# Kernel optimization log

Measured on AMD Instinct MI355X. Metric: run time of the kernel, lower is better.

The kernel has to match this reference:

```python
import jax, jax.numpy as jnp
import numpy as np

SIZE = 768
SMALL = SIZE // 4 + 1  # 193
N_ROWS = 16 * 512      # 8192 flattened timesteps
N_CODES = 30000
N_PAIRS = 300000


def setup_inputs() -> dict:
    key = jax.random.key(0)
    ks = jax.random.split(key, 10)
    rnn_output = jax.random.normal(ks[0], (16, 512, SIZE), dtype=jnp.float32)
    weight = jax.random.normal(ks[1], (N_CODES, SIZE + 1), dtype=jnp.float32) * 0.02
    weight1 = jax.random.normal(ks[2], (N_CODES, SMALL), dtype=jnp.float32) * 0.02
    idx0 = jnp.stack([
        jax.random.randint(ks[3], (N_PAIRS,), 0, N_ROWS),
        jax.random.randint(ks[4], (N_PAIRS,), 0, N_CODES),
    ], axis=1).astype(jnp.int64)
    y0 = (jax.random.uniform(ks[5], (N_PAIRS,)) < 0.5).astype(jnp.float32)
    idx1 = jnp.stack([
        jax.random.randint(ks[6], (N_PAIRS,), 0, N_ROWS),
        jax.random.randint(ks[7], (N_PAIRS,), 0, N_CODES),
    ], axis=1).astype(jnp.int64)
    y1 = (jax.random.uniform(ks[8], (N_PAIRS,)) < 0.5).astype(jnp.float32)
    seen0 = jnp.zeros((N_PAIRS,), dtype=jnp.float32)
    seen1 = jnp.zeros((N_PAIRS,), dtype=jnp.float32)
    return {"rnn_output": rnn_output, "weight": weight, "weight1": weight1,
            "idx0": idx0, "y0": y0, "seen0": seen0,
            "idx1": idx1, "y1": y1, "seen1": seen1}


def _embedding_dot(features, table, idx):
    # gather feature rows and code-embedding rows, then row-wise dot -> [N]
    f = features[idx[:, 0]]   # [N, D]
    w = table[idx[:, 1]]      # [N, D]
    return jnp.sum(f * w, axis=-1)


def _bce_logits_sum(logits, targets):
    # stable: log(1 + exp(x)) - x*y, summed
    return jnp.sum(jnp.logaddexp(jnp.float32(0.0), logits) - logits * targets)


def reference(rnn_output, weight, weight1, idx0, y0, seen0, idx1, y1, seen1):
    flat = rnn_output.reshape(-1, SIZE)                     # [B*T, size]
    bias = jnp.ones((flat.shape[0], 1), dtype=flat.dtype)
    rnn_with_bias = jnp.concatenate([flat, bias], axis=1)   # [B*T, size+1]

    final = _embedding_dot(rnn_with_bias, weight, idx0)     # [N]
    loss = _bce_logits_sum(final, y0)

    smaller = rnn_with_bias[:, -SMALL:]                     # [B*T, small]
    final1 = _embedding_dot(smaller, weight1, idx1)         # [N]
    loss1 = _bce_logits_sum(final1, y1)

    return final, loss + loss1
```

## Files before the change

kernel.cpp:

```cpp
#include <hip/hip_runtime.h>
#include <hip/hip_fp16.h>

#define FSIZE   768
#define TW0     769
#define TW1     193
#define COL1    576
#define NPAIRS  300000
#define NCODES  30000
#define NROWS   8192
#define W1STRIDE 200
#define NCB     32768
#define NWAVES0 (NPAIRS / 16)
#define NB0     ((NWAVES0 + 3) / 4)
#define NB1     (NPAIRS / 32)
#define NPART   (NB0 + NB1)

#define SZ_FEAT16 (NROWS * FSIZE / 2)
#define SZ_W116   (NCODES * W1STRIDE / 2)

typedef _Float16 h2_t __attribute__((ext_vector_type(2)));

#if defined(__has_builtin)
# if __has_builtin(__builtin_amdgcn_fdot2)
#  define HAVE_FDOT2 1
# endif
#endif

__device__ __forceinline__ float fdot2f(h2_t a, h2_t b, float c) {
#ifdef HAVE_FDOT2
    return __builtin_amdgcn_fdot2(a, b, c, false);
#else
    return (float)a[0] * (float)b[0] + (float)a[1] * (float)b[1] + c;
#endif
}

__device__ __forceinline__ float loss_term(float x, float y) {
    float ax = fabsf(x);
    return fmaxf(x, 0.0f) + log1pf(__expf(-ax)) - x * y;
}

__device__ __forceinline__ float4 ld4u(const float* p) {
    float4 v; __builtin_memcpy(&v, p, 16); return v;
}

__device__ __forceinline__ float acc8(uint4 u, float4 wa, float4 wb, float s) {
    h2_t h0, h1, h2v, h3;
    __builtin_memcpy(&h0, &u.x, 4);
    __builtin_memcpy(&h1, &u.y, 4);
    __builtin_memcpy(&h2v, &u.z, 4);
    __builtin_memcpy(&h3, &u.w, 4);
    s += (float)h0[0] * wa.x; s += (float)h0[1] * wa.y;
    s += (float)h1[0] * wa.z; s += (float)h1[1] * wa.w;
    s += (float)h2v[0] * wb.x; s += (float)h2v[1] * wb.y;
    s += (float)h3[0] * wb.z; s += (float)h3[1] * wb.w;
    return s;
}

__device__ __forceinline__ float dot8hh(uint4 a, uint4 b, float s) {
    h2_t a0, a1, a2, a3, b0, b1, b2, b3;
    __builtin_memcpy(&a0, &a.x, 4); __builtin_memcpy(&a1, &a.y, 4);
    __builtin_memcpy(&a2, &a.z, 4); __builtin_memcpy(&a3, &a.w, 4);
    __builtin_memcpy(&b0, &b.x, 4); __builtin_memcpy(&b1, &b.y, 4);
    __builtin_memcpy(&b2, &b.z, 4); __builtin_memcpy(&b3, &b.w, 4);
    s = fdot2f(a0, b0, s); s = fdot2f(a1, b1, s);
    s = fdot2f(a2, b2, s); s = fdot2f(a3, b3, s);
    return s;
}

__global__ __launch_bounds__(256) void conv_feat_kernel(
    const float* __restrict__ in, __half* __restrict__ out, int* __restrict__ cnt)
{
    const int gid = blockIdx.x * 256 + threadIdx.x;
    const int i = gid * 4;
    if (i < NROWS * FSIZE) {
        float4 v = *(const float4*)(in + i);
        __half2* o = (__half2*)(out + i);
        o[0] = __floats2half2_rn(v.x, v.y);
        o[1] = __floats2half2_rn(v.z, v.w);
    }
    if (gid < NCB) cnt[gid] = 0;
}

__global__ __launch_bounds__(256) void conv_w1_hist_kernel(
    const float* __restrict__ w1, __half* __restrict__ out,
    const int* __restrict__ idx0, int* __restrict__ cnt)
{
    const int gid = blockIdx.x * 256 + threadIdx.x;
    const int i4 = gid * 4;
    if (i4 < NCODES * W1STRIDE) {
        const int c = i4 / W1STRIDE;
        const int e = i4 - c * W1STRIDE;
        const float* src = w1 + (size_t)c * TW1;
        float v0 = 0.f, v1 = 0.f, v2 = 0.f, v3 = 0.f;
        if (e + 3 < TW1) {
            float4 f = ld4u(src + e);
            v0 = f.x; v1 = f.y; v2 = f.z; v3 = f.w;
        } else {
            if (e     < TW1) v0 = src[e];
            if (e + 1 < TW1) v1 = src[e + 1];
            if (e + 2 < TW1) v2 = src[e + 2];
        }
        __half2* dst = (__half2*)(out + i4);
        dst[0] = __floats2half2_rn(v0, v1);
        dst[1] = __floats2half2_rn(v2, v3);
    }
    if (gid < NPAIRS) atomicAdd(&cnt[idx0[2 * gid + 1]], 1);
}

__global__ __launch_bounds__(256) void hist_kernel(const int* __restrict__ idx,
                                                   int* __restrict__ cnt) {
    int p = blockIdx.x * 256 + threadIdx.x;
    if (p < NPAIRS) atomicAdd(&cnt[idx[2 * p + 1]], 1);
}

__global__ __launch_bounds__(1024) void scan_kernel(const int* __restrict__ cnt,
                                                    int* __restrict__ cursor) {
    __shared__ int wsum[16];
    __shared__ int wbase[16];
    const int t = threadIdx.x;
    const int lane = t & 63, wv = t >> 6;
    const int4* c4 = (const int4*)cnt + t * 8;
    int4 v[8];
#pragma unroll
    for (int j = 0; j < 8; ++j) v[j] = c4[j];
    int loc[32];
    int s = 0;
#pragma unroll
    for (int j = 0; j < 8; ++j) {
        loc[4 * j + 0] = s; s += v[j].x;
        loc[4 * j + 1] = s; s += v[j].y;
        loc[4 * j + 2] = s; s += v[j].z;
        loc[4 * j + 3] = s; s += v[j].w;
    }
    int incl = s;
#pragma unroll
    for (int off = 1; off < 64; off <<= 1) {
        int u = __shfl_up(incl, off, 64);
        if (lane >= off) incl += u;
    }
    if (lane == 63) wsum[wv] = incl;
    __syncthreads();
    if (wv == 0 && lane < 16) {
        int mysum = wsum[lane];
        int winc = mysum;
#pragma unroll
        for (int off = 1; off < 16; off <<= 1) {
            int u = __shfl_up(winc, off, 64);
            if (lane >= off) winc += u;
        }
        wbase[lane] = winc - mysum;
    }
    __syncthreads();
    const int base = wbase[wv] + incl - s;
    int4* cu = (int4*)cursor + t * 8;
#pragma unroll
    for (int j = 0; j < 8; ++j)
        cu[j] = make_int4(base + loc[4 * j], base + loc[4 * j + 1],
                          base + loc[4 * j + 2], base + loc[4 * j + 3]);
}

__global__ __launch_bounds__(256) void scatter_kernel(
    const int* __restrict__ idx, const float* __restrict__ y,
    int* __restrict__ cursor, uint4* __restrict__ srec)
{
    int p = blockIdx.x * 256 + threadIdx.x;
    if (p < NPAIRS) {
        int r = idx[2 * p];
        int c = idx[2 * p + 1];
        int pos = atomicAdd(&cursor[c], 1);
        srec[pos] = make_uint4((unsigned)r, (unsigned)c, __float_as_uint(y[p]), (unsigned)p);
    }
}

template <bool W1H>
__global__ __launch_bounds__(256, 4) void main_kernel(
    const __half* __restrict__ feat16, const float* __restrict__ w0,
    const float* __restrict__ w1f, const __half* __restrict__ w116,
    const uint4* __restrict__ srec,
    const int* __restrict__ idx1, const float* __restrict__ y1,
    float* __restrict__ out_final, float* __restrict__ partial)
{
    __shared__ float bsum[4];
    const int lane = threadIdx.x & 63;
    const int wv   = threadIdx.x >> 6;
    float wavesum = 0.f;

    if (blockIdx.x < NB0) {
        const int wid = blockIdx.x * 4 + wv;
        if (wid < NWAVES0) {
            const int g = lane >> 4, sub = lane & 15;
            const uint4 rec = srec[wid * 16 + 4 * g + (sub & 3)];
            int prev_c = -1;
            float4 wc[12];
            float wb = 0.f;
            float lg = 0.f;
#pragma unroll
            for (int j = 0; j < 4; ++j) {
                const int src = (lane & 48) | j;
                const int r = __shfl((int)rec.x, src, 64);
                const int c = __shfl((int)rec.y, src, 64);
                if (c != prev_c) {
                    prev_c = c;
                    const float* wrow = w0 + (size_t)c * TW0 + 8 * sub;
#pragma unroll
                    for (int k = 0; k < 6; ++k) {
                        wc[2 * k]     = ld4u(wrow + 128 * k);
                        wc[2 * k + 1] = ld4u(wrow + 128 * k + 4);
                    }
                    wb = w0[(size_t)c * TW0 + FSIZE];
                }
                const __half* fr = feat16 + (size_t)r * FSIZE + 8 * sub;
                float s = 0.f;
#pragma unroll
                for (int k = 0; k < 6; ++k) {
                    uint4 u = *(const uint4*)(fr + 128 * k);
                    s = acc8(u, wc[2 * k], wc[2 * k + 1], s);
                }
                s += __shfl_xor(s, 8, 64);
                s += __shfl_xor(s, 4, 64);
                s += __shfl_xor(s, 2, 64);
                s += __shfl_xor(s, 1, 64);
                s += wb;
                lg = (sub == j) ? s : lg;
            }
            float ll = 0.f;
            if (sub < 4) {
                out_final[rec.w] = lg;
                ll = loss_term(lg, __uint_as_float(rec.z));
            }
#pragma unroll
            for (int m = 32; m; m >>= 1) ll += __shfl_xor(ll, m, 64);
            wavesum = ll;
        }
    } else {
        const int bid  = blockIdx.x - NB0;
        const int sub  = lane & 7;
        const int pair = (bid * 4 + wv) * 8 + (lane >> 3);
        const int r = idx1[2 * pair];
        const int c = idx1[2 * pair + 1];
        const __half* fr = feat16 + (size_t)r * FSIZE + COL1 + 8 * sub;
        float s = 0.f;
        float bias;
        if (W1H) {
            const __half* wr = w116 + (size_t)c * W1STRIDE + 8 * sub;
#pragma unroll
            for (int k = 0; k < 3; ++k) {
                uint4 uf = *(const uint4*)(fr + 64 * k);
                uint4 uw = *(const uint4*)(wr + 64 * k);
                s = dot8hh(uf, uw, s);
            }
            bias = __half2float(w116[(size_t)c * W1STRIDE + 192]);
        } else {
            const float* wr = w1f + (size_t)c * TW1 + 8 * sub;
#pragma unroll
            for (int k = 0; k < 3; ++k) {
                uint4 uf = *(const uint4*)(fr + 64 * k);
                s = acc8(uf, ld4u(wr + 64 * k), ld4u(wr + 64 * k + 4), s);
            }
            bias = w1f[(size_t)c * TW1 + 192];
        }
        s += __shfl_xor(s, 4, 64);
        s += __shfl_xor(s, 2, 64);
        s += __shfl_xor(s, 1, 64);
        float ll = (sub == 0) ? loss_term(s + bias, y1[pair]) : 0.f;
#pragma unroll
        for (int m = 32; m; m >>= 1) ll += __shfl_xor(ll, m, 64);
        wavesum = ll;
    }

    if (lane == 0) bsum[wv] = wavesum;
    __syncthreads();
    if (threadIdx.x == 0)
        partial[blockIdx.x] = bsum[0] + bsum[1] + bsum[2] + bsum[3];
}

__global__ __launch_bounds__(1024) void reduce_kernel(
    const float* __restrict__ partial, int n, float* __restrict__ out)
{
    __shared__ float sh[1024];
    float s = 0.0f;
    for (int i = threadIdx.x; i < n; i += 1024) s += partial[i];
    sh[threadIdx.x] = s;
    __syncthreads();
    for (int off = 512; off; off >>= 1) {
        if ((int)threadIdx.x < off) sh[threadIdx.x] += sh[threadIdx.x + off];
        __syncthreads();
    }
    if (threadIdx.x == 0) out[0] = sh[0];
}

__global__ __launch_bounds__(256) void task0_kernel(
    const float* __restrict__ feat, const float* __restrict__ wt,
    const int* __restrict__ idx, const float* __restrict__ y,
    float* __restrict__ out_final, float* __restrict__ partial)
{
    __shared__ float lsum[4];
    const int lane = threadIdx.x & 63;
    const int wv = threadIdx.x >> 6;
    const int pair = blockIdx.x * 4 + wv;
    const int r = idx[2 * pair];
    const int c = idx[2 * pair + 1];
    const float4* f4 = (const float4*)(feat + (size_t)r * FSIZE);
    const float* wrow = wt + (size_t)c * TW0;
    float s = 0.0f;
#pragma unroll
    for (int k = 0; k < 3; ++k) {
        const int j = lane + (k << 6);
        float4 f = f4[j];
        float4 w = ld4u(wrow + 4 * j);
        s += f.x * w.x + f.y * w.y + f.z * w.z + f.w * w.w;
    }
#pragma unroll
    for (int m = 32; m; m >>= 1) s += __shfl_xor(s, m, 64);
    if (lane == 0) {
        const float logit = s + wrow[FSIZE];
        out_final[pair] = logit;
        lsum[wv] = loss_term(logit, y[pair]);
    }
    __syncthreads();
    if (threadIdx.x == 0)
        partial[blockIdx.x] = lsum[0] + lsum[1] + lsum[2] + lsum[3];
}

__global__ __launch_bounds__(256) void task1_kernel(
    const float* __restrict__ feat, const float* __restrict__ wt,
    const int* __restrict__ idx, const float* __restrict__ y,
    float* __restrict__ partial)
{
    __shared__ float lsum[16];
    const int lane = threadIdx.x & 63;
    const int wv = threadIdx.x >> 6;
    const int sub = lane & 15;
    const int pg = lane >> 4;
    const int pair = (blockIdx.x * 4 + wv) * 4 + pg;
    const int r = idx[2 * pair];
    const int c = idx[2 * pair + 1];
    const float4* f4 = (const float4*)(feat + (size_t)r * FSIZE + COL1);
    const float* wrow = wt + (size_t)c * TW1;
    float s = 0.0f;
#pragma unroll
    for (int k = 0; k < 3; ++k) {
        const int j = sub + (k << 4);
        float4 f = f4[j];
        float4 w = ld4u(wrow + 4 * j);
        s += f.x * w.x + f.y * w.y + f.z * w.z + f.w * w.w;
    }
#pragma unroll
    for (int m = 8; m; m >>= 1) s += __shfl_xor(s, m, 64);
    if (sub == 0) {
        const float logit = s + wrow[TW1 - 1];
        lsum[wv * 4 + pg] = loss_term(logit, y[pair]);
    }
    __syncthreads();
    if (threadIdx.x == 0) {
        float t = 0.0f;
#pragma unroll
        for (int i = 0; i < 16; ++i) t += lsum[i];
        partial[blockIdx.x] = t;
    }
}

extern "C" void kernel_launch(void* const* d_in, const int* in_sizes, int n_in,
                              void* d_out, int out_size, void* d_ws, size_t ws_size,
                              hipStream_t stream) {
    const float* feat = (const float*)d_in[0];
    const float* w0   = (const float*)d_in[1];
    const float* w1   = (const float*)d_in[2];
    const int*   idx0 = (const int*)d_in[3];
    const float* y0   = (const float*)d_in[4];
    const int*   idx1 = (const int*)d_in[6];
    const float* y1   = (const float*)d_in[7];

    float* out = (float*)d_out;
    float* ws  = (float*)d_ws;

    const size_t commonU = (size_t)NCB * 2 + (size_t)NPAIRS * 4 + NPART + 64;
    const size_t needA = (SZ_FEAT16 + SZ_W116 + commonU) * 4;
    const size_t needB = (SZ_FEAT16 + commonU) * 4;

    if (ws_size >= needB) {
        const bool tierA = (ws_size >= needA);
        size_t off = 0;
        __half* feat16 = (__half*)(ws + off); off += SZ_FEAT16;
        __half* w116 = nullptr;
        if (tierA) { w116 = (__half*)(ws + off); off += SZ_W116; }
        int* cnt    = (int*)(ws + off); off += NCB;
        int* cursor = (int*)(ws + off); off += NCB;
        uint4* srec = (uint4*)(ws + off); off += (size_t)NPAIRS * 4;
        float* part = ws + off;

        conv_feat_kernel<<<NROWS * FSIZE / 4 / 256, 256, 0, stream>>>(feat, feat16, cnt);
        if (tierA)
            conv_w1_hist_kernel<<<(NCODES * W1STRIDE / 4 + 255) / 256, 256, 0, stream>>>(
                w1, w116, idx0, cnt);
        else
            hist_kernel<<<(NPAIRS + 255) / 256, 256, 0, stream>>>(idx0, cnt);
        scan_kernel<<<1, 1024, 0, stream>>>(cnt, cursor);
        scatter_kernel<<<(NPAIRS + 255) / 256, 256, 0, stream>>>(idx0, y0, cursor, srec);
        if (tierA)
            main_kernel<true><<<NB0 + NB1, 256, 0, stream>>>(
                feat16, w0, w1, w116, srec, idx1, y1, out, part);
        else
            main_kernel<false><<<NB0 + NB1, 256, 0, stream>>>(
                feat16, w0, w1, nullptr, srec, idx1, y1, out, part);
        reduce_kernel<<<1, 1024, 0, stream>>>(part, NPART, out + NPAIRS);
    } else {
        float* part = ws;
        const int nb0 = NPAIRS / 4;
        const int nb1 = NPAIRS / 16;
        task0_kernel<<<nb0, 256, 0, stream>>>(feat, w0, idx0, y0, out, part);
        task1_kernel<<<nb1, 256, 0, stream>>>(feat, w1, idx1, y1, part + nb0);
        reduce_kernel<<<1, 1024, 0, stream>>>(part, nb0 + nb1, out + NPAIRS);
    }
}
```

Baseline: 160.3 us.

## Convert weight table to fp16 and process 8 pairs per group in task0

Adds a new top workspace tier that converts the full 30000x768 weight table to fp16, with a separate bias array, fused with the histogram pass. A new main kernel gathers fp16 weight rows (half the bytes) and handles 8 sorted pairs per 16-lane group instead of 4, so a reused code row is loaded once for more pairs. It also swizzles the block order for task0. The cost is an extra conversion pass over the ~92MB weight table on every call, plus more workspace.

```diff
diff --git a/kernel.cpp b/kernel.cpp
--- a/kernel.cpp
+++ b/kernel.cpp
@@ -10,12 +10,19 @@
 #define NROWS   8192
 #define W1STRIDE 200
 #define NCB     32768
-#define NWAVES0 (NPAIRS / 16)
+
+#define NWAVES0 (NPAIRS / 32)
 #define NB0     ((NWAVES0 + 3) / 4)
+#define NB0Q    (NB0 / 8)
 #define NB1     (NPAIRS / 32)
 #define NPART   (NB0 + NB1)
 
+#define NWAVES0B (NPAIRS / 16)
+#define NB0B    ((NWAVES0B + 3) / 4)
+#define NPARTB  (NB0B + NB1)
+
 #define SZ_FEAT16 (NROWS * FSIZE / 2)
+#define SZ_W016   (NCODES * FSIZE / 2)
 #define SZ_W116   (NCODES * W1STRIDE / 2)
 
 typedef _Float16 h2_t __attribute__((ext_vector_type(2)));
@@ -81,9 +88,28 @@
     if (gid < NCB) cnt[gid] = 0;
 }
 
-__global__ __launch_bounds__(256) void conv_w1_hist_kernel(
-    const float* __restrict__ w1, __half* __restrict__ out,
-    const int* __restrict__ idx0, int* __restrict__ cnt)
+__global__ __launch_bounds__(256) void conv_w0_hist_kernel(
+    const float* __restrict__ w0, __half* __restrict__ w016,
+    float* __restrict__ b0f, const int* __restrict__ idx0, int* __restrict__ cnt)
+{
+    const int gid = blockIdx.x * 256 + threadIdx.x;
+    if (gid < NCODES * (FSIZE / 8)) {
+        const int c = gid / (FSIZE / 8);
+        const int e = (gid - c * (FSIZE / 8)) * 8;
+        const float* src = w0 + (size_t)c * TW0 + e;
+        float4 a = ld4u(src), b = ld4u(src + 4);
+        __half2* dst = (__half2*)(w016 + (size_t)c * FSIZE + e);
+        dst[0] = __floats2half2_rn(a.x, a.y);
+        dst[1] = __floats2half2_rn(a.z, a.w);
+        dst[2] = __floats2half2_rn(b.x, b.y);
+        dst[3] = __floats2half2_rn(b.z, b.w);
+        if (e == 0) b0f[c] = w0[(size_t)c * TW0 + FSIZE];
+    }
+    if (gid < NPAIRS) atomicAdd(&cnt[idx0[2 * gid + 1]], 1);
+}
+
+__global__ __launch_bounds__(256) void conv_w1_kernel(
+    const float* __restrict__ w1, __half* __restrict__ out)
 {
     const int gid = blockIdx.x * 256 + threadIdx.x;
     const int i4 = gid * 4;
@@ -104,6 +130,31 @@
         dst[0] = __floats2half2_rn(v0, v1);
         dst[1] = __floats2half2_rn(v2, v3);
     }
+}
+
+__global__ __launch_bounds__(256) void conv_w1_hist_kernel(
+    const float* __restrict__ w1, __half* __restrict__ out,
+    const int* __restrict__ idx0, int* __restrict__ cnt)
+{
+    const int gid = blockIdx.x * 256 + threadIdx.x;
+    const int i4 = gid * 4;
+    if (i4 < NCODES * W1STRIDE) {
+        const int c = i4 / W1STRIDE;
+        const int e = i4 - c * W1STRIDE;
+        const float* src = w1 + (size_t)c * TW1;
+        float v0 = 0.f, v1 = 0.f, v2 = 0.f, v3 = 0.f;
+        if (e + 3 < TW1) {
+            float4 f = ld4u(src + e);
+            v0 = f.x; v1 = f.y; v2 = f.z; v3 = f.w;
+        } else {
+            if (e     < TW1) v0 = src[e];
+            if (e + 1 < TW1) v1 = src[e + 1];
+            if (e + 2 < TW1) v2 = src[e + 2];
+        }
+        __half2* dst = (__half2*)(out + i4);
+        dst[0] = __floats2half2_rn(v0, v1);
+        dst[1] = __floats2half2_rn(v2, v3);
+    }
     if (gid < NPAIRS) atomicAdd(&cnt[idx0[2 * gid + 1]], 1);
 }
 
@@ -172,6 +223,94 @@
     }
 }
 
+__global__ __launch_bounds__(256) void main2_kernel(
+    const __half* __restrict__ feat16, const __half* __restrict__ w016,
+    const float* __restrict__ b0f, const __half* __restrict__ w116,
+    const uint4* __restrict__ srec,
+    const int* __restrict__ idx1, const float* __restrict__ y1,
+    float* __restrict__ out_final, float* __restrict__ partial)
+{
+    __shared__ float bsum[4];
+    const int lane = threadIdx.x & 63;
+    const int wv   = threadIdx.x >> 6;
+    float wavesum = 0.f;
+
+    if (blockIdx.x < NB0) {
+        const int work = (blockIdx.x & 7) * NB0Q + (blockIdx.x >> 3);
+        const int wid = work * 4 + wv;
+        if (wid < NWAVES0) {
+            const int g = lane >> 4, sub = lane & 15;
+            const uint4 rec = srec[wid * 32 + 8 * g + (sub & 7)];
+            int prev_c = -1;
+            uint4 wc[6];
+            float wb = 0.f, lg = 0.f;
+#pragma unroll
+            for (int j = 0; j < 8; ++j) {
+                const int src = (lane & 48) | j;
+                const int r = __shfl((int)rec.x, src, 64);
+                const int c = __shfl((int)rec.y, src, 64);
+                if (c != prev_c) {
+                    prev_c = c;
+                    const __half* wrow = w016 + (size_t)c * FSIZE + 8 * sub;
+#pragma unroll
+                    for (int k = 0; k < 6; ++k)
+                        wc[k] = *(const uint4*)(wrow + 128 * k);
+                    wb = b0f[c];
+                }
+                const __half* fr = feat16 + (size_t)r * FSIZE + 8 * sub;
+                float s = 0.f;
+#pragma unroll
+                for (int k = 0; k < 6; ++k) {
+                    uint4 u = *(const uint4*)(fr + 128 * k);
+                    s = dot8hh(u, wc[k], s);
+                }
+                s += __shfl_xor(s, 8, 64);
+                s += __shfl_xor(s, 4, 64);
+                s += __shfl_xor(s, 2, 64);
+                s += __shfl_xor(s, 1, 64);
+                s += wb;
+                lg = (sub == j) ? s : lg;
+            }
+            float ll = 0.f;
+            if (sub < 8) {
+                out_final[rec.w] = lg;
+                ll = loss_term(lg, __uint_as_float(rec.z));
+            }
+#pragma unroll
+            for (int m = 32; m; m >>= 1) ll += __shfl_xor(ll, m, 64);
+            wavesum = ll;
+        }
+    } else {
+        const int bid  = blockIdx.x - NB0;
+        const int sub  = lane & 7;
+        const int pair = (bid * 4 + wv) * 8 + (lane >> 3);
+        const int r = idx1[2 * pair];
+        const int c = idx1[2 * pair + 1];
+        const __half* fr = feat16 + (size_t)r * FSIZE + COL1 + 8 * sub;
+        const __half* wr = w116 + (size_t)c * W1STRIDE + 8 * sub;
+        float s = 0.f;
+#pragma unroll
+        for (int k = 0; k < 3; ++k) {
+            uint4 uf = *(const uint4*)(fr + 64 * k);
+            uint4 uw = *(const uint4*)(wr + 64 * k);
+            s = dot8hh(uf, uw, s);
+        }
+        float bias = __half2float(w116[(size_t)c * W1STRIDE + 192]);
+        s += __shfl_xor(s, 4, 64);
+        s += __shfl_xor(s, 2, 64);
+        s += __shfl_xor(s, 1, 64);
+        float ll = (sub == 0) ? loss_term(s + bias, y1[pair]) : 0.f;
+#pragma unroll
+        for (int m = 32; m; m >>= 1) ll += __shfl_xor(ll, m, 64);
+        wavesum = ll;
+    }
+
+    if (lane == 0) bsum[wv] = wavesum;
+    __syncthreads();
+    if (threadIdx.x == 0)
+        partial[blockIdx.x] = bsum[0] + bsum[1] + bsum[2] + bsum[3];
+}
+
 template <bool W1H>
 __global__ __launch_bounds__(256, 4) void main_kernel(
     const __half* __restrict__ feat16, const float* __restrict__ w0,
@@ -185,9 +324,9 @@
     const int wv   = threadIdx.x >> 6;
     float wavesum = 0.f;
 
-    if (blockIdx.x < NB0) {
+    if (blockIdx.x < NB0B) {
         const int wid = blockIdx.x * 4 + wv;
-        if (wid < NWAVES0) {
+        if (wid < NWAVES0B) {
             const int g = lane >> 4, sub = lane & 15;
             const uint4 rec = srec[wid * 16 + 4 * g + (sub & 3)];
             int prev_c = -1;
@@ -233,7 +372,7 @@
             wavesum = ll;
         }
     } else {
-        const int bid  = blockIdx.x - NB0;
+        const int bid  = blockIdx.x - NB0B;
         const int sub  = lane & 7;
         const int pair = (bid * 4 + wv) * 8 + (lane >> 3);
         const int r = idx1[2 * pair];
@@ -374,36 +513,57 @@
     float* out = (float*)d_out;
     float* ws  = (float*)d_ws;
 
-    const size_t commonU = (size_t)NCB * 2 + (size_t)NPAIRS * 4 + NPART + 64;
-    const size_t needA = (SZ_FEAT16 + SZ_W116 + commonU) * 4;
-    const size_t needB = (SZ_FEAT16 + commonU) * 4;
-
-    if (ws_size >= needB) {
-        const bool tierA = (ws_size >= needA);
+    const size_t commonU = (size_t)NCB * 2 + (size_t)NPAIRS * 4 + 64;
+    const size_t needA2 = (SZ_FEAT16 + SZ_W016 + SZ_W116 + NCODES + commonU + NPART) * 4;
+    const size_t needB  = (SZ_FEAT16 + SZ_W116 + commonU + NPARTB) * 4;
+    const size_t needB2 = (SZ_FEAT16 + commonU + NPARTB) * 4;
+
+    if (ws_size >= needA2) {
+        size_t off = 0;
+        __half* feat16 = (__half*)(ws + off); off += SZ_FEAT16;
+        __half* w016   = (__half*)(ws + off); off += SZ_W016;
+        __half* w116   = (__half*)(ws + off); off += SZ_W116;
+        float*  b0f    = ws + off;            off += NCODES;
+        int* cnt       = (int*)(ws + off);    off += NCB;
+        int* cursor    = (int*)(ws + off);    off += NCB;
+        uint4* srec    = (uint4*)(ws + off);  off += (size_t)NPAIRS * 4;
+        float* part    = ws + off;
+
+        conv_feat_kernel<<<NROWS * FSIZE / 4 / 256, 256, 0, stream>>>(feat, feat16, cnt);
+        conv_w0_hist_kernel<<<(NCODES * (FSIZE / 8) + 255) / 256, 256, 0, stream>>>(
+            w0, w016, b0f, idx0, cnt);
+        conv_w1_kernel<<<(NCODES * W1STRIDE / 4 + 255) / 256, 256, 0, stream>>>(w1, w116);
+        scan_kernel<<<1, 1024, 0, stream>>>(cnt, cursor);
+        scatter_kernel<<<(NPAIRS + 255) / 256, 256, 0, stream>>>(idx0, y0, cursor, srec);
+        main2_kernel<<<NB0 + NB1, 256, 0, stream>>>(
+            feat16, w016, b0f, w116, srec, idx1, y1, out, part);
+        reduce_kernel<<<1, 1024, 0, stream>>>(part, NPART, out + NPAIRS);
+    } else if (ws_size >= needB2) {
+        const bool tierB = (ws_size >= needB);
         size_t off = 0;
         __half* feat16 = (__half*)(ws + off); off += SZ_FEAT16;
         __half* w116 = nullptr;
-        if (tierA) { w116 = (__half*)(ws + off); off += SZ_W116; }
+        if (tierB) { w116 = (__half*)(ws + off); off += SZ_W116; }
         int* cnt    = (int*)(ws + off); off += NCB;
         int* cursor = (int*)(ws + off); off += NCB;
         uint4* srec = (uint4*)(ws + off); off += (size_t)NPAIRS * 4;
         float* part = ws + off;
 
         conv_feat_kernel<<<NROWS * FSIZE / 4 / 256, 256, 0, stream>>>(feat, feat16, cnt);
-        if (tierA)
+        if (tierB)
             conv_w1_hist_kernel<<<(NCODES * W1STRIDE / 4 + 255) / 256, 256, 0, stream>>>(
                 w1, w116, idx0, cnt);
         else
             hist_kernel<<<(NPAIRS + 255) / 256, 256, 0, stream>>>(idx0, cnt);
         scan_kernel<<<1, 1024, 0, stream>>>(cnt, cursor);
         scatter_kernel<<<(NPAIRS + 255) / 256, 256, 0, stream>>>(idx0, y0, cursor, srec);
-        if (tierA)
-            main_kernel<true><<<NB0 + NB1, 256, 0, stream>>>(
+        if (tierB)
+            main_kernel<true><<<NB0B + NB1, 256, 0, stream>>>(
                 feat16, w0, w1, w116, srec, idx1, y1, out, part);
         else
-            main_kernel<false><<<NB0 + NB1, 256, 0, stream>>>(
+            main_kernel<false><<<NB0B + NB1, 256, 0, stream>>>(
                 feat16, w0, w1, nullptr, srec, idx1, y1, out, part);
-        reduce_kernel<<<1, 1024, 0, stream>>>(part, NPART, out + NPAIRS);
+        reduce_kernel<<<1, 1024, 0, stream>>>(part, NPARTB, out + NPAIRS);
     } else {
         float* part = ws;
         const int nb0 = NPAIRS / 4;
```

After: 168.8 us. 1.05x slower.
